# Optimization experiments

Hardware: AMD Instinct MI355X
Metric: run time of the kernel (lower is better)

The kernel has to match this reference:

```python
import jax, jax.numpy as jnp
import numpy as np

D = 1024  # input_size
NORM = 1.0 / np.sqrt(D)


def setup_inputs() -> dict:
    key = jax.random.key(0)
    k_x, k_q, k_k, k_v = jax.random.split(key, 4)
    B, S = 4, 2048
    scale = 1.0 / np.sqrt(D)  # init ~ nn.Linear default magnitude
    return {
        "inputs": jax.random.normal(k_x, (B, S, D), dtype=jnp.float32),
        "Wq": jax.random.uniform(k_q, (D, D), jnp.float32, -scale, scale),
        "Wk": jax.random.uniform(k_k, (D, D), jnp.float32, -scale, scale),
        "Wv": jax.random.uniform(k_v, (D, D), jnp.float32, -scale, scale),
    }


def reference(inputs, Wq, Wk, Wv):
    # nn.Linear(x) = x @ W.T (no bias)
    Q = jnp.einsum("bsd,ed->bse", inputs, Wq)
    K = jnp.einsum("bsd,ed->bse", inputs, Wk)
    V = jnp.einsum("bsd,ed->bse", inputs, Wv)
    attn = jnp.einsum("bqe,bke->bqk", Q, K) * NORM  # [B,S,S]
    attn = jax.nn.softmax(attn, axis=2)
    return jnp.einsum("bqk,bke->bqe", attn, V)
```

## Files before the change

kernel.cpp:

```cpp
#include <hip/hip_runtime.h>

typedef __bf16 bf16_t;
typedef __bf16 bf16x8 __attribute__((ext_vector_type(8)));
typedef __bf16 bf16x4 __attribute__((ext_vector_type(4)));
typedef float  floatx4 __attribute__((ext_vector_type(4)));

#define BM 128
#define BN 128
#define BK 64

__device__ __forceinline__ void gload_lds16(const bf16_t* g, bf16_t* l) {
    __builtin_amdgcn_global_load_lds(
        (const __attribute__((address_space(1))) void*)g,
        (__attribute__((address_space(3))) void*)l,
        16, 0, 0);
}

template <typename OutT, bool TRANSC>
__global__ __launch_bounds__(256) void gemm_nt(
    const bf16_t* __restrict__ A, int lda, size_t batchA,
    const bf16_t* __restrict__ B, int ldb, size_t batchB,
    OutT* __restrict__ C, int ldc, size_t batchC,
    int K, float scale)
{
    __shared__ bf16_t sA[BM * BK];
    __shared__ bf16_t sB[BN * BK];

    A += (size_t)blockIdx.z * batchA;
    B += (size_t)blockIdx.z * batchB;
    C += (size_t)blockIdx.z * batchC;

    const int tid  = threadIdx.x;
    const int wid  = tid >> 6;
    const int lane = tid & 63;

    const int bm = blockIdx.x * BM;
    const int bn = blockIdx.y * BN;

    const int rr  = tid >> 3;
    const int kc8 = (((tid & 7) ^ (rr & 7)) << 3);

    const int wy = (wid >> 1) * 64;
    const int wx = (wid & 1) * 64;
    const int lr = lane & 15;

    floatx4 acc[4][4] = {};

    const bf16_t* pa = A + (size_t)(bm + rr) * lda + kc8;
    const bf16_t* pb = B + (size_t)(bn + rr) * ldb + kc8;
    bf16_t* la = &sA[wid * 512];
    bf16_t* lb = &sB[wid * 512];

    for (int k0 = 0; k0 < K; k0 += BK) {
        #pragma unroll
        for (int c = 0; c < 4; ++c) {
            gload_lds16(pa + (size_t)(c * 32) * lda + k0, la + c * 2048);
            gload_lds16(pb + (size_t)(c * 32) * ldb + k0, lb + c * 2048);
        }
        __syncthreads();

        #pragma unroll
        for (int kk = 0; kk < 2; ++kk) {
            const int cch = (kk << 2) + (lane >> 4);
            bf16x8 af[4], bq[4];
            #pragma unroll
            for (int i = 0; i < 4; ++i) {
                int r = wy + i * 16 + lr;
                af[i] = *(const bf16x8*)&sA[(r << 6) + ((cch ^ (r & 7)) << 3)];
            }
            #pragma unroll
            for (int j = 0; j < 4; ++j) {
                int r = wx + j * 16 + lr;
                bq[j] = *(const bf16x8*)&sB[(r << 6) + ((cch ^ (r & 7)) << 3)];
            }
            #pragma unroll
            for (int i = 0; i < 4; ++i)
                #pragma unroll
                for (int j = 0; j < 4; ++j) {
                    if constexpr (!TRANSC)
                        acc[i][j] = __builtin_amdgcn_mfma_f32_16x16x32_bf16(
                            bq[j], af[i], acc[i][j], 0, 0, 0);
                    else
                        acc[i][j] = __builtin_amdgcn_mfma_f32_16x16x32_bf16(
                            af[i], bq[j], acc[i][j], 0, 0, 0);
                }
        }
        __syncthreads();
    }

    const int cfix = lane & 15;
    const int creg = (lane >> 4) << 2;
    #pragma unroll
    for (int i = 0; i < 4; ++i)
        #pragma unroll
        for (int j = 0; j < 4; ++j) {
            size_t row; int col;
            if constexpr (!TRANSC) {
                row = (size_t)(bm + wy + i * 16 + cfix);
                col = bn + wx + j * 16 + creg;
            } else {
                row = (size_t)(bn + wx + j * 16 + cfix);
                col = bm + wy + i * 16 + creg;
            }
            if constexpr (sizeof(OutT) == 2) {
                bf16x4 v;
                #pragma unroll
                for (int r = 0; r < 4; ++r) v[r] = (bf16_t)(acc[i][j][r] * scale);
                *(bf16x4*)&C[row * (size_t)ldc + col] = v;
            } else {
                floatx4 v = acc[i][j] * scale;
                *(floatx4*)&C[row * (size_t)ldc + col] = v;
            }
        }
}

__global__ __launch_bounds__(256) void cvt_all(
    const float* __restrict__ X, const float* __restrict__ Wq,
    const float* __restrict__ Wk, const float* __restrict__ Wv,
    bf16_t* __restrict__ Xb, bf16_t* __restrict__ Wqb,
    bf16_t* __restrict__ Wkb, bf16_t* __restrict__ Wvb,
    int nX4, int nW4)
{
    int i = blockIdx.x * blockDim.x + threadIdx.x;
    const float* src; bf16_t* dst; int idx;
    if (i < nX4) { src = X; dst = Xb; idx = i; }
    else {
        int j = i - nX4;
        int w = j / nW4;
        idx = j - w * nW4;
        if (i >= nX4 + 3 * nW4) return;
        src = (w == 0) ? Wq : (w == 1) ? Wk : Wv;
        dst = (w == 0) ? Wqb : (w == 1) ? Wkb : Wvb;
    }
    float4 v = ((const float4*)src)[idx];
    bf16x4 o;
    o[0] = (bf16_t)v.x; o[1] = (bf16_t)v.y; o[2] = (bf16_t)v.z; o[3] = (bf16_t)v.w;
    *(bf16x4*)(dst + (size_t)idx * 4) = o;
}

__global__ __launch_bounds__(256) void softmax_inplace(bf16_t* __restrict__ S, int ncols)
{
    __shared__ float red[4];
    bf16_t* p = S + (size_t)blockIdx.x * ncols;
    const int t = threadIdx.x;

    bf16x8 raw = *(const bf16x8*)&p[t * 8];
    float v[8];
    #pragma unroll
    for (int r = 0; r < 8; ++r) v[r] = (float)raw[r];

    float m = v[0];
    #pragma unroll
    for (int r = 1; r < 8; ++r) m = fmaxf(m, v[r]);
    #pragma unroll
    for (int off = 32; off >= 1; off >>= 1) m = fmaxf(m, __shfl_xor(m, off));
    if ((t & 63) == 0) red[t >> 6] = m;
    __syncthreads();
    m = fmaxf(fmaxf(red[0], red[1]), fmaxf(red[2], red[3]));
    __syncthreads();

    float e[8], s = 0.f;
    #pragma unroll
    for (int r = 0; r < 8; ++r) { e[r] = __expf(v[r] - m); s += e[r]; }
    #pragma unroll
    for (int off = 32; off >= 1; off >>= 1) s += __shfl_xor(s, off);
    if ((t & 63) == 0) red[t >> 6] = s;
    __syncthreads();
    s = red[0] + red[1] + red[2] + red[3];

    float inv = 1.0f / s;
    bf16x8 o;
    #pragma unroll
    for (int r = 0; r < 8; ++r) o[r] = (bf16_t)(e[r] * inv);
    *(bf16x8*)&p[t * 8] = o;
}

extern "C" void kernel_launch(void* const* d_in, const int* in_sizes, int n_in,
                              void* d_out, int out_size, void* d_ws, size_t ws_size,
                              hipStream_t stream)
{
    (void)in_sizes; (void)n_in; (void)out_size; (void)ws_size;
    const float* X  = (const float*)d_in[0];
    const float* Wq = (const float*)d_in[1];
    const float* Wk = (const float*)d_in[2];
    const float* Wv = (const float*)d_in[3];
    float* out = (float*)d_out;

    const int Bb = 4, S = 2048, D = 1024;
    const int M = Bb * S;

    char* ws = (char*)d_ws;
    size_t off = 0;
    auto carve = [&](size_t bytes) -> char* {
        char* p = ws + off;
        off += (bytes + 255) & ~(size_t)255;
        return p;
    };
    bf16_t* Xb  = (bf16_t*)carve((size_t)M * D * 2);
    bf16_t* Wqb = (bf16_t*)carve((size_t)D * D * 2);
    bf16_t* Wkb = (bf16_t*)carve((size_t)D * D * 2);
    bf16_t* Wvb = (bf16_t*)carve((size_t)D * D * 2);
    bf16_t* Qb  = (bf16_t*)carve((size_t)M * D * 2);
    bf16_t* Kb  = (bf16_t*)carve((size_t)M * D * 2);
    bf16_t* Vt  = (bf16_t*)carve((size_t)D * M * 2);
    bf16_t* Sc  = (bf16_t*)carve((size_t)Bb * S * S * 2);

    const int nX4 = M * D / 4, nW4 = D * D / 4;
    const int tot4 = nX4 + 3 * nW4;
    cvt_all<<<(tot4 + 255) / 256, 256, 0, stream>>>(
        X, Wq, Wk, Wv, Xb, Wqb, Wkb, Wvb, nX4, nW4);

    gemm_nt<bf16_t, false><<<dim3(M / BM, D / BN, 2), 256, 0, stream>>>(
        Xb, D, 0, Wqb, D, (size_t)D * D, Qb, D, (size_t)M * D, D, 1.0f);

    gemm_nt<bf16_t, true><<<dim3(M / BM, D / BN, 1), 256, 0, stream>>>(
        Xb, D, 0, Wvb, D, 0, Vt, M, 0, D, 1.0f);

    gemm_nt<bf16_t, false><<<dim3(S / BM, S / BN, Bb), 256, 0, stream>>>(
        Qb, D, (size_t)S * D, Kb, D, (size_t)S * D, Sc, S, (size_t)S * S,
        D, 0.03125f);

    softmax_inplace<<<Bb * S, 256, 0, stream>>>(Sc, S);

    gemm_nt<float, false><<<dim3(S / BM, D / BN, Bb), 256, 0, stream>>>(
        Sc, S, (size_t)S * S, Vt, M, (size_t)S, out, D, (size_t)S * D,
        S, 1.0f);
}
```

Measured before the change: 277.9 us.

## Switch GEMMs to 32x32x16 MFMA with templated M-tile and larger tiles

Replaces the 16x16x32 MFMA inner loop with 32x32x16 MFMA instructions, each accumulating into a 16-float register tile. The M-tile becomes a template parameter, so the QK projection and score GEMMs use 256x128 blocks. The V-transpose GEMM now swaps its operands instead of using a transposed-store path. The larger MFMA shape and tiles aim to cut LDS fragment reads per FLOP and raise per-block reuse, at the cost of more accumulator registers and fewer blocks per GEMM.

```diff
diff --git a/kernel.cpp b/kernel.cpp
--- a/kernel.cpp
+++ b/kernel.cpp
@@ -3,10 +3,9 @@
 typedef __bf16 bf16_t;
 typedef __bf16 bf16x8 __attribute__((ext_vector_type(8)));
 typedef __bf16 bf16x4 __attribute__((ext_vector_type(4)));
-typedef float  floatx4 __attribute__((ext_vector_type(4)));
-
-#define BM 128
-#define BN 128
+typedef float  floatx4  __attribute__((ext_vector_type(4)));
+typedef float  floatx16 __attribute__((ext_vector_type(16)));
+
 #define BK 64
 
 __device__ __forceinline__ void gload_lds16(const bf16_t* g, bf16_t* l) {
@@ -16,15 +15,15 @@
         16, 0, 0);
 }
 
-template <typename OutT, bool TRANSC>
+template <typename OutT, int MT>
 __global__ __launch_bounds__(256) void gemm_nt(
     const bf16_t* __restrict__ A, int lda, size_t batchA,
     const bf16_t* __restrict__ B, int ldb, size_t batchB,
     OutT* __restrict__ C, int ldc, size_t batchC,
     int K, float scale)
 {
-    __shared__ bf16_t sA[BM * BK];
-    __shared__ bf16_t sB[BN * BK];
+    __shared__ bf16_t sA[64 * MT * BK];
+    __shared__ bf16_t sB[128 * BK];
 
     A += (size_t)blockIdx.z * batchA;
     B += (size_t)blockIdx.z * batchB;
@@ -34,17 +33,18 @@
     const int wid  = tid >> 6;
     const int lane = tid & 63;
 
-    const int bm = blockIdx.x * BM;
-    const int bn = blockIdx.y * BN;
+    const int bm = blockIdx.x * (64 * MT);
+    const int bn = blockIdx.y * 128;
 
     const int rr  = tid >> 3;
     const int kc8 = (((tid & 7) ^ (rr & 7)) << 3);
 
-    const int wy = (wid >> 1) * 64;
-    const int wx = (wid & 1) * 64;
-    const int lr = lane & 15;
-
-    floatx4 acc[4][4] = {};
+    const int wyy = (wid >> 1) * (32 * MT);
+    const int wxx = (wid & 1) * 64;
+    const int lrow = lane & 31;
+    const int khalf = lane >> 5;
+
+    floatx16 acc[MT][2] = {};
 
     const bf16_t* pa = A + (size_t)(bm + rr) * lda + kc8;
     const bf16_t* pb = B + (size_t)(bn + rr) * ldb + kc8;
@@ -53,63 +53,60 @@
 
     for (int k0 = 0; k0 < K; k0 += BK) {
         #pragma unroll
-        for (int c = 0; c < 4; ++c) {
+        for (int c = 0; c < 2 * MT; ++c)
             gload_lds16(pa + (size_t)(c * 32) * lda + k0, la + c * 2048);
+        #pragma unroll
+        for (int c = 0; c < 4; ++c)
             gload_lds16(pb + (size_t)(c * 32) * ldb + k0, lb + c * 2048);
-        }
         __syncthreads();
 
         #pragma unroll
-        for (int kk = 0; kk < 2; ++kk) {
-            const int cch = (kk << 2) + (lane >> 4);
-            bf16x8 af[4], bq[4];
-            #pragma unroll
-            for (int i = 0; i < 4; ++i) {
-                int r = wy + i * 16 + lr;
+        for (int ks = 0; ks < 4; ++ks) {
+            const int cch = (ks << 1) | khalf;
+            bf16x8 af[MT], bq[2];
+            #pragma unroll
+            for (int i = 0; i < MT; ++i) {
+                int r = wyy + i * 32 + lrow;
                 af[i] = *(const bf16x8*)&sA[(r << 6) + ((cch ^ (r & 7)) << 3)];
             }
             #pragma unroll
-            for (int j = 0; j < 4; ++j) {
-                int r = wx + j * 16 + lr;
+            for (int j = 0; j < 2; ++j) {
+                int r = wxx + j * 32 + lrow;
                 bq[j] = *(const bf16x8*)&sB[(r << 6) + ((cch ^ (r & 7)) << 3)];
             }
             #pragma unroll
-            for (int i = 0; i < 4; ++i)
+            for (int i = 0; i < MT; ++i)
                 #pragma unroll
-                for (int j = 0; j < 4; ++j) {
-                    if constexpr (!TRANSC)
-                        acc[i][j] = __builtin_amdgcn_mfma_f32_16x16x32_bf16(
-                            bq[j], af[i], acc[i][j], 0, 0, 0);
-                    else
-                        acc[i][j] = __builtin_amdgcn_mfma_f32_16x16x32_bf16(
-                            af[i], bq[j], acc[i][j], 0, 0, 0);
-                }
+                for (int j = 0; j < 2; ++j)
+                    acc[i][j] = __builtin_amdgcn_mfma_f32_32x32x16_bf16(
+                        bq[j], af[i], acc[i][j], 0, 0, 0);
         }
         __syncthreads();
     }
 
-    const int cfix = lane & 15;
-    const int creg = (lane >> 4) << 2;
-    #pragma unroll
-    for (int i = 0; i < 4; ++i)
-        #pragma unroll
-        for (int j = 0; j < 4; ++j) {
-            size_t row; int col;
-            if constexpr (!TRANSC) {
-                row = (size_t)(bm + wy + i * 16 + cfix);
-                col = bn + wx + j * 16 + creg;
-            } else {
-                row = (size_t)(bn + wx + j * 16 + cfix);
-                col = bm + wy + i * 16 + creg;
-            }
-            if constexpr (sizeof(OutT) == 2) {
-                bf16x4 v;
-                #pragma unroll
-                for (int r = 0; r < 4; ++r) v[r] = (bf16_t)(acc[i][j][r] * scale);
-                *(bf16x4*)&C[row * (size_t)ldc + col] = v;
-            } else {
-                floatx4 v = acc[i][j] * scale;
-                *(floatx4*)&C[row * (size_t)ldc + col] = v;
+    const int m_off = lrow;
+    const int n_off = khalf << 2;
+    #pragma unroll
+    for (int i = 0; i < MT; ++i)
+        #pragma unroll
+        for (int j = 0; j < 2; ++j) {
+            size_t row = (size_t)(bm + wyy + i * 32 + m_off);
+            #pragma unroll
+            for (int g = 0; g < 4; ++g) {
+                int col = bn + wxx + j * 32 + g * 8 + n_off;
+                if constexpr (sizeof(OutT) == 2) {
+                    bf16x4 v;
+                    #pragma unroll
+                    for (int r = 0; r < 4; ++r)
+                        v[r] = (bf16_t)(acc[i][j][g * 4 + r] * scale);
+                    *(bf16x4*)&C[row * (size_t)ldc + col] = v;
+                } else {
+                    floatx4 v;
+                    #pragma unroll
+                    for (int r = 0; r < 4; ++r)
+                        v[r] = acc[i][j][g * 4 + r] * scale;
+                    *(floatx4*)&C[row * (size_t)ldc + col] = v;
+                }
             }
         }
 }
@@ -210,19 +207,19 @@
     cvt_all<<<(tot4 + 255) / 256, 256, 0, stream>>>(
         X, Wq, Wk, Wv, Xb, Wqb, Wkb, Wvb, nX4, nW4);
 
-    gemm_nt<bf16_t, false><<<dim3(M / BM, D / BN, 2), 256, 0, stream>>>(
+    gemm_nt<bf16_t, 4><<<dim3(M / 256, D / 128, 2), 256, 0, stream>>>(
         Xb, D, 0, Wqb, D, (size_t)D * D, Qb, D, (size_t)M * D, D, 1.0f);
 
-    gemm_nt<bf16_t, true><<<dim3(M / BM, D / BN, 1), 256, 0, stream>>>(
-        Xb, D, 0, Wvb, D, 0, Vt, M, 0, D, 1.0f);
-
-    gemm_nt<bf16_t, false><<<dim3(S / BM, S / BN, Bb), 256, 0, stream>>>(
+    gemm_nt<bf16_t, 2><<<dim3(D / 128, M / 128, 1), 256, 0, stream>>>(
+        Wvb, D, 0, Xb, D, 0, Vt, M, 0, D, 1.0f);
+
+    gemm_nt<bf16_t, 4><<<dim3(S / 256, S / 128, Bb), 256, 0, stream>>>(
         Qb, D, (size_t)S * D, Kb, D, (size_t)S * D, Sc, S, (size_t)S * S,
         D, 0.03125f);
 
     softmax_inplace<<<Bb * S, 256, 0, stream>>>(Sc, S);
 
-    gemm_nt<float, false><<<dim3(S / BM, D / BN, Bb), 256, 0, stream>>>(
+    gemm_nt<float, 2><<<dim3(S / 128, D / 128, Bb), 256, 0, stream>>>(
         Sc, S, (size_t)S * S, Vt, M, (size_t)S, out, D, (size_t)S * D,
         S, 1.0f);
 }
```

Measured after the change: 295.1 us. +6.2%, slower.

## Fuse exp into QK^T epilogue, defer softmax normalization to PV GEMM

Applied to the files above, without the earlier changes.

The QKV projections now run as one 3-slice launch, with the V slice writing its transpose using scalar strided stores. The QK^T GEMM epilogue applies exp directly without subtracting the row max, and the old softmax kernel becomes a lightweight row-sum pass producing reciprocals. The final PV GEMM scales each output row by its reciprocal. This removes one read-modify-write pass over the score matrix and one launch. The cost is dropping max-subtraction, which risks overflow for large scores, plus uncoalesced scalar stores for V^T.

```diff
diff --git a/kernel.cpp b/kernel.cpp
--- a/kernel.cpp
+++ b/kernel.cpp
@@ -16,11 +16,13 @@
         16, 0, 0);
 }
 
-template <typename OutT, bool TRANSC>
+template <int MODE, typename OutT>
 __global__ __launch_bounds__(256) void gemm_nt(
     const bf16_t* __restrict__ A, int lda, size_t batchA,
     const bf16_t* __restrict__ B, int ldb, size_t batchB,
     OutT* __restrict__ C, int ldc, size_t batchC,
+    bf16_t* __restrict__ C2, int ldc2,
+    const float* __restrict__ rowinv, int batchR,
     int K, float scale)
 {
     __shared__ bf16_t sA[BM * BK];
@@ -28,7 +30,6 @@
 
     A += (size_t)blockIdx.z * batchA;
     B += (size_t)blockIdx.z * batchB;
-    C += (size_t)blockIdx.z * batchC;
 
     const int tid  = threadIdx.x;
     const int wid  = tid >> 6;
@@ -76,42 +77,77 @@
             #pragma unroll
             for (int i = 0; i < 4; ++i)
                 #pragma unroll
-                for (int j = 0; j < 4; ++j) {
-                    if constexpr (!TRANSC)
-                        acc[i][j] = __builtin_amdgcn_mfma_f32_16x16x32_bf16(
-                            bq[j], af[i], acc[i][j], 0, 0, 0);
-                    else
-                        acc[i][j] = __builtin_amdgcn_mfma_f32_16x16x32_bf16(
-                            af[i], bq[j], acc[i][j], 0, 0, 0);
-                }
+                for (int j = 0; j < 4; ++j)
+                    acc[i][j] = __builtin_amdgcn_mfma_f32_16x16x32_bf16(
+                        bq[j], af[i], acc[i][j], 0, 0, 0);
         }
         __syncthreads();
     }
 
     const int cfix = lane & 15;
     const int creg = (lane >> 4) << 2;
-    #pragma unroll
-    for (int i = 0; i < 4; ++i)
-        #pragma unroll
-        for (int j = 0; j < 4; ++j) {
-            size_t row; int col;
-            if constexpr (!TRANSC) {
-                row = (size_t)(bm + wy + i * 16 + cfix);
-                col = bn + wx + j * 16 + creg;
-            } else {
-                row = (size_t)(bn + wx + j * 16 + cfix);
-                col = bm + wy + i * 16 + creg;
-            }
-            if constexpr (sizeof(OutT) == 2) {
+
+    if constexpr (MODE == 1) {
+        if (blockIdx.z == 2) {
+            #pragma unroll
+            for (int i = 0; i < 4; ++i) {
+                int mg = bm + wy + i * 16 + cfix;
+                #pragma unroll
+                for (int j = 0; j < 4; ++j) {
+                    int ng = bn + wx + j * 16 + creg;
+                    #pragma unroll
+                    for (int r = 0; r < 4; ++r)
+                        C2[(size_t)(ng + r) * ldc2 + mg] = (bf16_t)acc[i][j][r];
+                }
+            }
+            return;
+        }
+        OutT* Cz = C + (size_t)blockIdx.z * batchC;
+        #pragma unroll
+        for (int i = 0; i < 4; ++i) {
+            size_t row = (size_t)(bm + wy + i * 16 + cfix);
+            #pragma unroll
+            for (int j = 0; j < 4; ++j) {
+                int col = bn + wx + j * 16 + creg;
                 bf16x4 v;
                 #pragma unroll
-                for (int r = 0; r < 4; ++r) v[r] = (bf16_t)(acc[i][j][r] * scale);
-                *(bf16x4*)&C[row * (size_t)ldc + col] = v;
-            } else {
-                floatx4 v = acc[i][j] * scale;
-                *(floatx4*)&C[row * (size_t)ldc + col] = v;
-            }
-        }
+                for (int r = 0; r < 4; ++r) v[r] = (bf16_t)acc[i][j][r];
+                *(bf16x4*)&Cz[row * (size_t)ldc + col] = v;
+            }
+        }
+    } else if constexpr (MODE == 2) {
+        OutT* Cz = C + (size_t)blockIdx.z * batchC;
+        #pragma unroll
+        for (int i = 0; i < 4; ++i) {
+            size_t row = (size_t)(bm + wy + i * 16 + cfix);
+            #pragma unroll
+            for (int j = 0; j < 4; ++j) {
+                int col = bn + wx + j * 16 + creg;
+                bf16x4 v;
+                #pragma unroll
+                for (int r = 0; r < 4; ++r)
+                    v[r] = (bf16_t)__expf(acc[i][j][r] * scale);
+                *(bf16x4*)&Cz[row * (size_t)ldc + col] = v;
+            }
+        }
+    } else {
+        OutT* Cz = C + (size_t)blockIdx.z * batchC;
+        const float* rz = rowinv + (size_t)blockIdx.z * batchR;
+        #pragma unroll
+        for (int i = 0; i < 4; ++i) {
+            int rloc = bm + wy + i * 16 + cfix;
+            float rinv = rz[rloc];
+            size_t row = (size_t)rloc;
+            #pragma unroll
+            for (int j = 0; j < 4; ++j) {
+                int col = bn + wx + j * 16 + creg;
+                floatx4 v;
+                #pragma unroll
+                for (int r = 0; r < 4; ++r) v[r] = acc[i][j][r] * rinv;
+                *(floatx4*)&Cz[row * (size_t)ldc + col] = v;
+            }
+        }
+    }
 }
 
 __global__ __launch_bounds__(256) void cvt_all(
@@ -138,41 +174,22 @@
     *(bf16x4*)(dst + (size_t)idx * 4) = o;
 }
 
-__global__ __launch_bounds__(256) void softmax_inplace(bf16_t* __restrict__ S, int ncols)
-{
-    __shared__ float red[4];
-    bf16_t* p = S + (size_t)blockIdx.x * ncols;
-    const int t = threadIdx.x;
-
-    bf16x8 raw = *(const bf16x8*)&p[t * 8];
-    float v[8];
+__global__ __launch_bounds__(256) void rowsum_inv(
+    const bf16_t* __restrict__ Sc, float* __restrict__ inv)
+{
+    const int row  = blockIdx.x * 4 + (threadIdx.x >> 6);
+    const int lane = threadIdx.x & 63;
+    const bf16_t* p = Sc + (size_t)row * 2048;
+    float s = 0.f;
     #pragma unroll
-    for (int r = 0; r < 8; ++r) v[r] = (float)raw[r];
-
-    float m = v[0];
-    #pragma unroll
-    for (int r = 1; r < 8; ++r) m = fmaxf(m, v[r]);
-    #pragma unroll
-    for (int off = 32; off >= 1; off >>= 1) m = fmaxf(m, __shfl_xor(m, off));
-    if ((t & 63) == 0) red[t >> 6] = m;
-    __syncthreads();
-    m = fmaxf(fmaxf(red[0], red[1]), fmaxf(red[2], red[3]));
-    __syncthreads();
-
-    float e[8], s = 0.f;
-    #pragma unroll
-    for (int r = 0; r < 8; ++r) { e[r] = __expf(v[r] - m); s += e[r]; }
+    for (int c = 0; c < 4; ++c) {
+        bf16x8 v = *(const bf16x8*)&p[c * 512 + lane * 8];
+        #pragma unroll
+        for (int r = 0; r < 8; ++r) s += (float)v[r];
+    }
     #pragma unroll
     for (int off = 32; off >= 1; off >>= 1) s += __shfl_xor(s, off);
-    if ((t & 63) == 0) red[t >> 6] = s;
-    __syncthreads();
-    s = red[0] + red[1] + red[2] + red[3];
-
-    float inv = 1.0f / s;
-    bf16x8 o;
-    #pragma unroll
-    for (int r = 0; r < 8; ++r) o[r] = (bf16_t)(e[r] * inv);
-    *(bf16x8*)&p[t * 8] = o;
+    if (lane == 0) inv[row] = 1.0f / s;
 }
 
 extern "C" void kernel_launch(void* const* d_in, const int* in_sizes, int n_in,
@@ -204,25 +221,24 @@
     bf16_t* Kb  = (bf16_t*)carve((size_t)M * D * 2);
     bf16_t* Vt  = (bf16_t*)carve((size_t)D * M * 2);
     bf16_t* Sc  = (bf16_t*)carve((size_t)Bb * S * S * 2);
+    float*  inv = (float*)carve((size_t)M * 4);
 
     const int nX4 = M * D / 4, nW4 = D * D / 4;
     const int tot4 = nX4 + 3 * nW4;
     cvt_all<<<(tot4 + 255) / 256, 256, 0, stream>>>(
         X, Wq, Wk, Wv, Xb, Wqb, Wkb, Wvb, nX4, nW4);
 
-    gemm_nt<bf16_t, false><<<dim3(M / BM, D / BN, 2), 256, 0, stream>>>(
-        Xb, D, 0, Wqb, D, (size_t)D * D, Qb, D, (size_t)M * D, D, 1.0f);
-
-    gemm_nt<bf16_t, true><<<dim3(M / BM, D / BN, 1), 256, 0, stream>>>(
-        Xb, D, 0, Wvb, D, 0, Vt, M, 0, D, 1.0f);
-
-    gemm_nt<bf16_t, false><<<dim3(S / BM, S / BN, Bb), 256, 0, stream>>>(
+    gemm_nt<1, bf16_t><<<dim3(M / BM, D / BN, 3), 256, 0, stream>>>(
+        Xb, D, 0, Wqb, D, (size_t)D * D, Qb, D, (size_t)M * D,
+        Vt, M, nullptr, 0, D, 1.0f);
+
+    gemm_nt<2, bf16_t><<<dim3(S / BM, S / BN, Bb), 256, 0, stream>>>(
         Qb, D, (size_t)S * D, Kb, D, (size_t)S * D, Sc, S, (size_t)S * S,
-        D, 0.03125f);
-
-    softmax_inplace<<<Bb * S, 256, 0, stream>>>(Sc, S);
-
-    gemm_nt<float, false><<<dim3(S / BM, D / BN, Bb), 256, 0, stream>>>(
+        nullptr, 0, nullptr, 0, D, 0.03125f);
+
+    rowsum_inv<<<Bb * S / 4, 256, 0, stream>>>(Sc, inv);
+
+    gemm_nt<3, float><<<dim3(S / BM, D / BN, Bb), 256, 0, stream>>>(
         Sc, S, (size_t)S * S, Vt, M, (size_t)S, out, D, (size_t)S * D,
-        S, 1.0f);
-}
+        nullptr, 0, inv, S, S, 1.0f);
+}
```

New measurement: 244.7 us. -11.9%, faster.
